# Performance work log

Hardware: AMD Instinct MI355X
Metric: run time of the kernel (lower is better)

Reference implementation:

```python
import jax, jax.numpy as jnp
import numpy as np

N_NODES = 50000


def setup_inputs() -> dict:
    key = jax.random.key(0)
    k1, k2, k3, k4, k5 = jax.random.split(key, 5)
    x = jax.random.normal(k1, (N_NODES, 256), dtype=jnp.float32)
    edge_row = jax.random.randint(k2, (800000,), 0, N_NODES, dtype=jnp.int32)
    edge_col = jax.random.randint(k3, (800000,), 0, N_NODES, dtype=jnp.int32)
    edge_val = jax.random.uniform(k4, (800000,), dtype=jnp.float32)
    W = jax.random.normal(k5, (256, 256), dtype=jnp.float32) * 0.0625  # ~1/sqrt(256)
    b = jnp.zeros((256,), dtype=jnp.float32)
    return {"x": x, "edge_row": edge_row, "edge_col": edge_col,
            "edge_val": edge_val, "W": W, "b": b}


def reference(x, edge_row, edge_col, edge_val, W, b):
    # SpMM: agg[i] = sum_{e: row(e)=i} val(e) * x[col(e)]
    msgs = edge_val[:, None] * x[edge_col]                      # [E, F_in]
    agg = jax.ops.segment_sum(msgs, edge_row, num_segments=N_NODES)  # [N, F_in]
    # nn.Linear: agg @ W.T + b
    return jnp.einsum('nf,of->no', agg, W) + b
```

## Files before the change

kernel.cpp:

```cpp
#include <hip/hip_runtime.h>

typedef unsigned short u16;
typedef __attribute__((ext_vector_type(8))) short short8;
typedef __attribute__((ext_vector_type(4))) float f32x4;
typedef __attribute__((ext_vector_type(4))) u16 u16x4;

#define F 256

__device__ __forceinline__ u16 f2bf(float f) {
  unsigned u = __float_as_uint(f);
  unsigned r = u + 0x7fffu + ((u >> 16) & 1u);
  return (u16)(r >> 16);
}

__device__ __forceinline__ f32x4 bf4_to_f32(u16x4 u) {
  f32x4 x;
#pragma unroll
  for (int j = 0; j < 4; j++) x[j] = __uint_as_float((unsigned)u[j] << 16);
  return x;
}

__global__ void zero_int(int* __restrict__ p, int n) {
  int i = blockIdx.x * 256 + threadIdx.x;
  if (i < n) p[i] = 0;
}

__global__ void hist_k(const int* __restrict__ erow, int* __restrict__ off, int E) {
  int e = blockIdx.x * 256 + threadIdx.x;
  if (e < E) atomicAdd(&off[erow[e] + 1], 1);
}

__global__ void scan1_k(int* __restrict__ a, int* __restrict__ blks, int n) {
  __shared__ int s[256];
  int t = threadIdx.x;
  int i = blockIdx.x * 256 + t;
  s[t] = (i < n) ? a[i] : 0;
  __syncthreads();
  for (int d = 1; d < 256; d <<= 1) {
    int v = (t >= d) ? s[t - d] : 0;
    __syncthreads();
    s[t] += v;
    __syncthreads();
  }
  if (i < n) a[i] = s[t];
  if (t == 255) blks[blockIdx.x] = s[255];
}

__global__ void scan2_k(int* __restrict__ blks, int nb) {
  __shared__ int s[256];
  int t = threadIdx.x;
  s[t] = (t < nb) ? blks[t] : 0;
  __syncthreads();
  for (int d = 1; d < 256; d <<= 1) {
    int v = (t >= d) ? s[t - d] : 0;
    __syncthreads();
    s[t] += v;
    __syncthreads();
  }
  if (t < nb) blks[t] = (t == 0) ? 0 : s[t - 1];
}

__global__ void scan3_k(int* __restrict__ a, const int* __restrict__ blks,
                        int* __restrict__ cur, int n, int nn) {
  int i = blockIdx.x * 256 + threadIdx.x;
  if (i < n) {
    int v = a[i] + blks[blockIdx.x];
    a[i] = v;
    if (i < nn) cur[i] = v;
  }
}

__global__ void scatter_k(const int* __restrict__ erow, const int* __restrict__ ecol,
                          const float* __restrict__ eval, int* __restrict__ cur,
                          int2* __restrict__ epk, int E) {
  int e = blockIdx.x * 256 + threadIdx.x;
  if (e < E) {
    int r = erow[e];
    int p = atomicAdd(&cur[r], 1);
    epk[p] = make_int2(ecol[e], __float_as_int(eval[e]));
  }
}

__global__ void convw_k(const float* __restrict__ src, u16* __restrict__ dst, int n) {
  int i = blockIdx.x * 256 + threadIdx.x;
  if (i < n) dst[i] = f2bf(src[i]);
}

__global__ void __launch_bounds__(256, 2) gemm_k(const float* __restrict__ x,
                                                 const u16* __restrict__ wb,
                                                 u16* __restrict__ yb,
                                                 int NT, int stride) {
  int w = (int)(threadIdx.x >> 6);
  int lane = threadIdx.x & 63;
  int ln = lane & 15, q = lane >> 4;

  short8 Bf[4][8];
#pragma unroll
  for (int j = 0; j < 4; j++) {
#pragma unroll
    for (int t = 0; t < 8; t++) {
      Bf[j][t] = *(const short8*)(wb + (size_t)((4 * w + j) * 16 + ln) * F + t * 32 + q * 8);
    }
  }

  for (int mt = blockIdx.x; mt < NT; mt += stride) {
    const float* arow = x + (size_t)(mt * 16 + ln) * F + q * 8;
    f32x4 acc[4];
#pragma unroll
    for (int j = 0; j < 4; j++) acc[j] = (f32x4){0.f, 0.f, 0.f, 0.f};

#pragma unroll
    for (int t = 0; t < 8; t++) {
      const f32x4* a4 = (const f32x4*)(arow + t * 32);
      f32x4 alo = a4[0], ahi = a4[1];
      short8 a;
#pragma unroll
      for (int j = 0; j < 4; j++) {
        a[j]     = (short)f2bf(alo[j]);
        a[4 + j] = (short)f2bf(ahi[j]);
      }
#pragma unroll
      for (int j = 0; j < 4; j++) {
        acc[j] = __builtin_amdgcn_mfma_f32_16x16x32_bf16(a, Bf[j][t], acc[j], 0, 0, 0);
      }
    }

    int m0 = mt * 16;
#pragma unroll
    for (int j = 0; j < 4; j++) {
#pragma unroll
      for (int r = 0; r < 4; r++) {
        yb[(size_t)(m0 + q * 4 + r) * F + (4 * w + j) * 16 + ln] = f2bf(acc[j][r]);
      }
    }
  }
}

__global__ void __launch_bounds__(256) gather_k(const int* __restrict__ off,
                                                const int2* __restrict__ epk,
                                                const u16* __restrict__ yb,
                                                const float* __restrict__ bias,
                                                float* __restrict__ out, int NN) {
  int wave = (int)((blockIdx.x * 256 + threadIdx.x) >> 6);
  int lane = threadIdx.x & 63;
  if (wave >= NN) return;
  int s = off[wave], e = off[wave + 1];

  f32x4 acc0 = ((const f32x4*)bias)[lane];
  f32x4 acc1 = (f32x4){0.f, 0.f, 0.f, 0.f};
  f32x4 acc2 = (f32x4){0.f, 0.f, 0.f, 0.f};
  f32x4 acc3 = (f32x4){0.f, 0.f, 0.f, 0.f};

  int k = s;
  for (; k + 4 <= e; k += 4) {
    int2 p0 = epk[k], p1 = epk[k + 1], p2 = epk[k + 2], p3 = epk[k + 3];
    u16x4 u0 = *(const u16x4*)(yb + (size_t)p0.x * F + lane * 4);
    u16x4 u1 = *(const u16x4*)(yb + (size_t)p1.x * F + lane * 4);
    u16x4 u2 = *(const u16x4*)(yb + (size_t)p2.x * F + lane * 4);
    u16x4 u3 = *(const u16x4*)(yb + (size_t)p3.x * F + lane * 4);
    acc0 += __int_as_float(p0.y) * bf4_to_f32(u0);
    acc1 += __int_as_float(p1.y) * bf4_to_f32(u1);
    acc2 += __int_as_float(p2.y) * bf4_to_f32(u2);
    acc3 += __int_as_float(p3.y) * bf4_to_f32(u3);
  }
  for (; k < e; k++) {
    int2 p = epk[k];
    u16x4 u = *(const u16x4*)(yb + (size_t)p.x * F + lane * 4);
    acc0 += __int_as_float(p.y) * bf4_to_f32(u);
  }
  acc0 += acc1;
  acc2 += acc3;
  acc0 += acc2;
  ((f32x4*)out)[(size_t)wave * 64 + lane] = acc0;
}

extern "C" void kernel_launch(void* const* d_in, const int* in_sizes, int n_in,
                              void* d_out, int out_size, void* d_ws, size_t ws_size,
                              hipStream_t stream) {
  const float* x    = (const float*)d_in[0];
  const int*   erow = (const int*)d_in[1];
  const int*   ecol = (const int*)d_in[2];
  const float* eval = (const float*)d_in[3];
  const float* Wm   = (const float*)d_in[4];
  const float* bias = (const float*)d_in[5];
  float* out = (float*)d_out;

  int NN = in_sizes[0] / F;
  int E  = in_sizes[1];

  char* base = (char*)d_ws;
  size_t o = 0;
  auto carve = [&](size_t bytes) {
    void* p = base + o;
    o += (bytes + 255) & ~(size_t)255;
    return p;
  };
  u16*   yb   = (u16*)carve((size_t)NN * F * 2);
  u16*   wb   = (u16*)carve((size_t)F * F * 2);
  int*   off  = (int*)carve((size_t)(NN + 1) * 4);
  int*   cur  = (int*)carve((size_t)NN * 4);
  int*   blks = (int*)carve(256 * 4);
  int2*  epk  = (int2*)carve((size_t)E * 8);

  int nOff  = NN + 1;
  int nbOff = (nOff + 255) / 256;
  int nbE   = (E + 255) / 256;

  zero_int<<<nbOff, 256, 0, stream>>>(off, nOff);
  hist_k<<<nbE, 256, 0, stream>>>(erow, off, E);
  scan1_k<<<nbOff, 256, 0, stream>>>(off, blks, nOff);
  scan2_k<<<1, 256, 0, stream>>>(blks, nbOff);
  scan3_k<<<nbOff, 256, 0, stream>>>(off, blks, cur, nOff, NN);
  scatter_k<<<nbE, 256, 0, stream>>>(erow, ecol, eval, cur, epk, E);

  convw_k<<<(F * F + 255) / 256, 256, 0, stream>>>(Wm, wb, F * F);
  int NT = (NN + 15) / 16;
  int nBlocks = 512;
  gemm_k<<<nBlocks, 256, 0, stream>>>(x, wb, yb, NT, nBlocks);

  gather_k<<<(NN + 3) / 4, 256, 0, stream>>>(off, epk, yb, bias, out, NN);
}
```

Before: 298.2 us.

## Cut launches by fusing scan stages, inlining W conversion, and deepen gather unroll

Replaces the zeroing kernel with hipMemsetAsync. Merges the second and third scan kernels so each block recomputes the block-sum prefix in shared memory. Removes the separate weight-to-bf16 kernel by converting W inside the GEMM prologue. Unrolls the gather loop from 4 to 8 edges with more accumulators. Together these aim to cut launch overhead and expose more memory-level parallelism in the gather, at the cost of redundant prefix and weight conversion work per block and higher register pressure.

```diff
diff --git a/kernel.cpp b/kernel.cpp
--- a/kernel.cpp
+++ b/kernel.cpp
@@ -20,17 +20,12 @@
   return x;
 }
 
-__global__ void zero_int(int* __restrict__ p, int n) {
-  int i = blockIdx.x * 256 + threadIdx.x;
-  if (i < n) p[i] = 0;
-}
-
 __global__ void hist_k(const int* __restrict__ erow, int* __restrict__ off, int E) {
   int e = blockIdx.x * 256 + threadIdx.x;
   if (e < E) atomicAdd(&off[erow[e] + 1], 1);
 }
 
-__global__ void scan1_k(int* __restrict__ a, int* __restrict__ blks, int n) {
+__global__ void scanA_k(int* __restrict__ a, int* __restrict__ blks, int n) {
   __shared__ int s[256];
   int t = threadIdx.x;
   int i = blockIdx.x * 256 + t;
@@ -46,7 +41,8 @@
   if (t == 255) blks[blockIdx.x] = s[255];
 }
 
-__global__ void scan2_k(int* __restrict__ blks, int nb) {
+__global__ void scanB_k(int* __restrict__ a, const int* __restrict__ blks,
+                        int* __restrict__ cur, int n, int nn, int nb) {
   __shared__ int s[256];
   int t = threadIdx.x;
   s[t] = (t < nb) ? blks[t] : 0;
@@ -57,14 +53,10 @@
     s[t] += v;
     __syncthreads();
   }
-  if (t < nb) blks[t] = (t == 0) ? 0 : s[t - 1];
-}
-
-__global__ void scan3_k(int* __restrict__ a, const int* __restrict__ blks,
-                        int* __restrict__ cur, int n, int nn) {
-  int i = blockIdx.x * 256 + threadIdx.x;
+  int prefix = (blockIdx.x == 0) ? 0 : s[blockIdx.x - 1];
+  int i = blockIdx.x * 256 + t;
   if (i < n) {
-    int v = a[i] + blks[blockIdx.x];
+    int v = a[i] + prefix;
     a[i] = v;
     if (i < nn) cur[i] = v;
   }
@@ -81,13 +73,8 @@
   }
 }
 
-__global__ void convw_k(const float* __restrict__ src, u16* __restrict__ dst, int n) {
-  int i = blockIdx.x * 256 + threadIdx.x;
-  if (i < n) dst[i] = f2bf(src[i]);
-}
-
 __global__ void __launch_bounds__(256, 2) gemm_k(const float* __restrict__ x,
-                                                 const u16* __restrict__ wb,
+                                                 const float* __restrict__ Wm,
                                                  u16* __restrict__ yb,
                                                  int NT, int stride) {
   int w = (int)(threadIdx.x >> 6);
@@ -99,7 +86,15 @@
   for (int j = 0; j < 4; j++) {
 #pragma unroll
     for (int t = 0; t < 8; t++) {
-      Bf[j][t] = *(const short8*)(wb + (size_t)((4 * w + j) * 16 + ln) * F + t * 32 + q * 8);
+      const f32x4* wp = (const f32x4*)(Wm + (size_t)((4 * w + j) * 16 + ln) * F + t * 32 + q * 8);
+      f32x4 wlo = wp[0], whi = wp[1];
+      short8 bfrag;
+#pragma unroll
+      for (int i = 0; i < 4; i++) {
+        bfrag[i]     = (short)f2bf(wlo[i]);
+        bfrag[4 + i] = (short)f2bf(whi[i]);
+      }
+      Bf[j][t] = bfrag;
     }
   }
 
@@ -150,27 +145,40 @@
   f32x4 acc1 = (f32x4){0.f, 0.f, 0.f, 0.f};
   f32x4 acc2 = (f32x4){0.f, 0.f, 0.f, 0.f};
   f32x4 acc3 = (f32x4){0.f, 0.f, 0.f, 0.f};
+  f32x4 acc4 = (f32x4){0.f, 0.f, 0.f, 0.f};
+  f32x4 acc5 = (f32x4){0.f, 0.f, 0.f, 0.f};
+  f32x4 acc6 = (f32x4){0.f, 0.f, 0.f, 0.f};
+  f32x4 acc7 = (f32x4){0.f, 0.f, 0.f, 0.f};
 
   int k = s;
-  for (; k + 4 <= e; k += 4) {
-    int2 p0 = epk[k], p1 = epk[k + 1], p2 = epk[k + 2], p3 = epk[k + 3];
+  for (; k + 8 <= e; k += 8) {
+    int2 p0 = epk[k],     p1 = epk[k + 1], p2 = epk[k + 2], p3 = epk[k + 3];
+    int2 p4 = epk[k + 4], p5 = epk[k + 5], p6 = epk[k + 6], p7 = epk[k + 7];
     u16x4 u0 = *(const u16x4*)(yb + (size_t)p0.x * F + lane * 4);
     u16x4 u1 = *(const u16x4*)(yb + (size_t)p1.x * F + lane * 4);
     u16x4 u2 = *(const u16x4*)(yb + (size_t)p2.x * F + lane * 4);
     u16x4 u3 = *(const u16x4*)(yb + (size_t)p3.x * F + lane * 4);
+    u16x4 u4 = *(const u16x4*)(yb + (size_t)p4.x * F + lane * 4);
+    u16x4 u5 = *(const u16x4*)(yb + (size_t)p5.x * F + lane * 4);
+    u16x4 u6 = *(const u16x4*)(yb + (size_t)p6.x * F + lane * 4);
+    u16x4 u7 = *(const u16x4*)(yb + (size_t)p7.x * F + lane * 4);
     acc0 += __int_as_float(p0.y) * bf4_to_f32(u0);
     acc1 += __int_as_float(p1.y) * bf4_to_f32(u1);
     acc2 += __int_as_float(p2.y) * bf4_to_f32(u2);
     acc3 += __int_as_float(p3.y) * bf4_to_f32(u3);
+    acc4 += __int_as_float(p4.y) * bf4_to_f32(u4);
+    acc5 += __int_as_float(p5.y) * bf4_to_f32(u5);
+    acc6 += __int_as_float(p6.y) * bf4_to_f32(u6);
+    acc7 += __int_as_float(p7.y) * bf4_to_f32(u7);
   }
   for (; k < e; k++) {
     int2 p = epk[k];
     u16x4 u = *(const u16x4*)(yb + (size_t)p.x * F + lane * 4);
     acc0 += __int_as_float(p.y) * bf4_to_f32(u);
   }
-  acc0 += acc1;
-  acc2 += acc3;
-  acc0 += acc2;
+  acc0 += acc1; acc2 += acc3; acc4 += acc5; acc6 += acc7;
+  acc0 += acc2; acc4 += acc6;
+  acc0 += acc4;
   ((f32x4*)out)[(size_t)wave * 64 + lane] = acc0;
 }
 
@@ -196,7 +204,6 @@
     return p;
   };
   u16*   yb   = (u16*)carve((size_t)NN * F * 2);
-  u16*   wb   = (u16*)carve((size_t)F * F * 2);
   int*   off  = (int*)carve((size_t)(NN + 1) * 4);
   int*   cur  = (int*)carve((size_t)NN * 4);
   int*   blks = (int*)carve(256 * 4);
@@ -206,17 +213,15 @@
   int nbOff = (nOff + 255) / 256;
   int nbE   = (E + 255) / 256;
 
-  zero_int<<<nbOff, 256, 0, stream>>>(off, nOff);
+  hipMemsetAsync(off, 0, (size_t)nOff * 4, stream);
   hist_k<<<nbE, 256, 0, stream>>>(erow, off, E);
-  scan1_k<<<nbOff, 256, 0, stream>>>(off, blks, nOff);
-  scan2_k<<<1, 256, 0, stream>>>(blks, nbOff);
-  scan3_k<<<nbOff, 256, 0, stream>>>(off, blks, cur, nOff, NN);
+  scanA_k<<<nbOff, 256, 0, stream>>>(off, blks, nOff);
+  scanB_k<<<nbOff, 256, 0, stream>>>(off, blks, cur, nOff, NN, nbOff);
   scatter_k<<<nbE, 256, 0, stream>>>(erow, ecol, eval, cur, epk, E);
 
-  convw_k<<<(F * F + 255) / 256, 256, 0, stream>>>(Wm, wb, F * F);
   int NT = (NN + 15) / 16;
   int nBlocks = 512;
-  gemm_k<<<nBlocks, 256, 0, stream>>>(x, wb, yb, NT, nBlocks);
+  gemm_k<<<nBlocks, 256, 0, stream>>>(x, Wm, yb, NT, nBlocks);
 
   gather_k<<<(NN + 3) / 4, 256, 0, stream>>>(off, epk, yb, bias, out, NN);
 }
```

Result: slower. 309.3 us (+3.7%).
